# Performance work log

Measured on AMD Instinct MI355X. Metric: run time of the kernel, lower is better.

The kernel has to match this reference:

```python
import jax, jax.numpy as jnp
import numpy as np

N_NODES = 100000
IN_DIM = 128
HID = 128
N_REL = 2
N_EDGES = 500000


def setup_inputs() -> dict:
    key = jax.random.key(0)
    ks = jax.random.split(key, 12)
    x = jax.random.normal(ks[0], (N_NODES, IN_DIM), dtype=jnp.float32)
    edge_index = jax.random.randint(ks[1], (2, N_EDGES), 0, N_NODES, dtype=jnp.int64)
    edge_type = jax.random.randint(ks[2], (N_EDGES,), 0, N_REL, dtype=jnp.int64)
    def w(k, shape, fan_in):
        return jax.random.normal(k, shape, dtype=jnp.float32) / np.sqrt(fan_in)
    return {
        "x": x,
        "edge_index": edge_index,
        "edge_type": edge_type,
        "W_rel1": w(ks[3], (N_REL, IN_DIM, HID), IN_DIM),
        "W_root1": w(ks[4], (IN_DIM, HID), IN_DIM),
        "b1": jnp.zeros((HID,), jnp.float32),
        "W_rel2": w(ks[5], (N_REL, HID, HID), HID),
        "W_root2": w(ks[6], (HID, HID), HID),
        "b2": jnp.zeros((HID,), jnp.float32),
        "Wc": w(ks[7], (HID, 2), HID),
        "bc": jnp.zeros((2,), jnp.float32),
    }


def rgcn_conv(x, src, dst, edge_type, W_rel, W_root, b, n_nodes):
    """PyG RGCNConv: out_i = x_i @ W_root + b + sum_r mean_{j in N_r(i)} x_j @ W_r."""
    out = x @ W_root + b
    for r in range(W_rel.shape[0]):  # small fixed relation count
        mask = (edge_type == r).astype(x.dtype)  # [E]
        xr = x @ W_rel[r]                         # [N, dout] transform-then-gather
        msg = xr[src] * mask[:, None]             # [E, dout]
        agg = jax.ops.segment_sum(msg, dst, num_segments=n_nodes)   # [N, dout]
        cnt = jax.ops.segment_sum(mask, dst, num_segments=n_nodes)  # [N]
        out = out + agg / jnp.maximum(cnt, 1.0)[:, None]            # mean aggr
    return out


def reference(x, edge_index, edge_type, W_rel1, W_root1, b1, W_rel2, W_root2, b2, Wc, bc):
    n = x.shape[0]
    src, dst = edge_index[0], edge_index[1]
    h = rgcn_conv(x, src, dst, edge_type, W_rel1, W_root1, b1, n)
    h = jax.nn.relu(h)
    # dropout is identity at inference (training=False)
    h = rgcn_conv(h, src, dst, edge_type, W_rel2, W_root2, b2, n)
    h = jax.nn.relu(h)
    logits = h @ Wc + bc
    return logits
```

## Files before the change

### kernel.cpp

```cpp
#include <hip/hip_runtime.h>
#include <hip/hip_fp16.h>

#define N_NODES 100000
#define PAD_N   100096
#define IN_DIM 128
#define HID 128
#define N_REL 2
#define N_EDGES 500000
#define M_SEG (N_REL * N_NODES)
#define SCAN_BLK 1024
#define SCAN_NB ((M_SEG + SCAN_BLK - 1) / SCAN_BLK)

#define CVT_BLOCKS 12500
#define PACK_BLOCKS 48
#define HIST_BLOCKS 1954

typedef __attribute__((ext_vector_type(8))) _Float16 half8;
typedef __attribute__((ext_vector_type(4))) float float4v;

__device__ __forceinline__ unsigned short f2h(float f) {
    return __half_as_ushort(__float2half(f));
}

__global__ __launch_bounds__(256) void prep_kernel(
    const float* __restrict__ X, unsigned short* __restrict__ Xb,
    const float* __restrict__ Wroot1, const float* __restrict__ Wrel1,
    const float* __restrict__ Wroot2, const float* __restrict__ Wrel2,
    unsigned short* __restrict__ Wp,
    const int* __restrict__ ei, const int* __restrict__ et,
    unsigned* __restrict__ cnt)
{
    int bid = blockIdx.x;
    if (bid < CVT_BLOCKS) {
        int i = bid * 256 + threadIdx.x;
        if (i >= N_NODES * IN_DIM / 4) return;
        float4 v = ((const float4*)X)[i];
        ushort4 o;
        o.x = f2h(v.x); o.y = f2h(v.y); o.z = f2h(v.z); o.w = f2h(v.w);
        ((ushort4*)Xb)[i] = o;
    } else if (bid < CVT_BLOCKS + PACK_BLOCKS) {
        int tid = (bid - CVT_BLOCKS) * 256 + threadIdx.x;
        int layer = tid / 6144;
        int rem   = tid % 6144;
        int ks    = rem / 512;
        int rem2  = rem % 512;
        int nt    = rem2 / 64;
        int lane  = rem2 % 64;
        int seg = ks >> 2;
        int kl  = (ks & 3) * 32 + (lane >> 4) * 8;
        int chan = nt * 16 + (lane & 15);
        const float* Wroot = layer ? Wroot2 : Wroot1;
        const float* Wrel  = layer ? Wrel2  : Wrel1;
        const float* W = (seg == 0) ? Wroot : (Wrel + (size_t)(seg - 1) * 128 * 128);
        unsigned short* dst = Wp + (size_t)tid * 8;
        #pragma unroll
        for (int j = 0; j < 8; ++j)
            dst[j] = f2h(W[(size_t)(kl + j) * 128 + chan]);
    } else {
        int e = (bid - CVT_BLOCKS - PACK_BLOCKS) * 256 + threadIdx.x;
        if (e >= N_EDGES) return;
        int dst = ei[N_EDGES + e];
        int r = et[e];
        atomicAdd(cnt + (size_t)r * N_NODES + dst, 1u);
    }
}

__global__ __launch_bounds__(256) void scan1_kernel(
    const unsigned* __restrict__ cnt,
    unsigned* __restrict__ rs, unsigned* __restrict__ bsums)
{
    __shared__ unsigned sdata[256];
    int t = threadIdx.x;
    int base = blockIdx.x * SCAN_BLK + t * 4;
    unsigned v[4]; unsigned s = 0;
    #pragma unroll
    for (int j = 0; j < 4; ++j) {
        v[j] = (base + j < M_SEG) ? cnt[base + j] : 0u;
        s += v[j];
    }
    sdata[t] = s;
    __syncthreads();
    #pragma unroll
    for (int off = 1; off < 256; off <<= 1) {
        unsigned x = (t >= off) ? sdata[t - off] : 0u;
        __syncthreads();
        if (t >= off) sdata[t] += x;
        __syncthreads();
    }
    unsigned excl = (t > 0) ? sdata[t - 1] : 0u;
    if (t == 255) bsums[blockIdx.x] = sdata[255];
    unsigned run = excl;
    #pragma unroll
    for (int j = 0; j < 4; ++j) {
        if (base + j < M_SEG) rs[base + j] = run;
        run += v[j];
    }
}

__global__ __launch_bounds__(256) void scan2_kernel(unsigned* __restrict__ bsums)
{
    __shared__ unsigned sdata[256];
    int t = threadIdx.x;
    sdata[t] = (t < SCAN_NB) ? bsums[t] : 0u;
    __syncthreads();
    #pragma unroll
    for (int off = 1; off < 256; off <<= 1) {
        unsigned x = (t >= off) ? sdata[t - off] : 0u;
        __syncthreads();
        if (t >= off) sdata[t] += x;
        __syncthreads();
    }
    if (t < SCAN_NB) bsums[t] = (t > 0) ? sdata[t - 1] : 0u;
}

__global__ __launch_bounds__(256) void scan3_kernel(
    unsigned* __restrict__ rs, const unsigned* __restrict__ bsums,
    unsigned* __restrict__ cursor)
{
    int i = blockIdx.x * blockDim.x + threadIdx.x;
    if (i < M_SEG) {
        unsigned v = rs[i] + bsums[i >> 10];
        rs[i] = v;
        cursor[i] = v;
    }
    if (i == 0) rs[M_SEG] = N_EDGES;
}

__global__ __launch_bounds__(256) void fill_kernel(
    const int* __restrict__ ei, const int* __restrict__ et,
    unsigned* __restrict__ cursor, unsigned* __restrict__ csr)
{
    int e = blockIdx.x * blockDim.x + threadIdx.x;
    if (e >= N_EDGES) return;
    int src = ei[e];
    int dst = ei[N_EDGES + e];
    int r = et[e];
    unsigned pos = atomicAdd(cursor + (size_t)r * N_NODES + dst, 1u);
    csr[pos] = (unsigned)src;
}

__global__ __launch_bounds__(256) void gather_kernel(
    const unsigned short* __restrict__ Xb,
    const unsigned* __restrict__ rs,
    const unsigned* __restrict__ csr,
    unsigned short* __restrict__ agg)
{
    int t = blockIdx.x * blockDim.x + threadIdx.x;
    int seg = t >> 5;
    int lane = t & 31;
    if (seg >= M_SEG) return;
    const int e2  = lane >> 4;
    const int c16 = lane & 15;

    unsigned start = rs[seg];
    unsigned end   = rs[seg + 1];

    const uint4* __restrict__ X4 = (const uint4*)Xb;

    __half2 acc[4];
    #pragma unroll
    for (int j = 0; j < 4; ++j) acc[j] = __float2half2_rn(0.f);

    for (unsigned p = start + e2; p < end; p += 2) {
        unsigned s = csr[p];
        uint4 v = X4[(s << 4) | (unsigned)c16];
        acc[0] = __hadd2(acc[0], *(const __half2*)&v.x);
        acc[1] = __hadd2(acc[1], *(const __half2*)&v.y);
        acc[2] = __hadd2(acc[2], *(const __half2*)&v.z);
        acc[3] = __hadd2(acc[3], *(const __half2*)&v.w);
    }

    #pragma unroll
    for (int j = 0; j < 4; ++j) {
        int other = __shfl_xor(*(const int*)&acc[j], 16, 32);
        acc[j] = __hadd2(acc[j], *(const __half2*)&other);
    }

    if (e2 == 0) {
        unsigned c = end - start;
        float scale = 1.0f / (float)(c > 0u ? c : 1u);
        __half2 s2 = __float2half2_rn(scale);
        uint4 o;
        __half2 r0 = __hmul2(acc[0], s2);
        __half2 r1 = __hmul2(acc[1], s2);
        __half2 r2 = __hmul2(acc[2], s2);
        __half2 r3 = __hmul2(acc[3], s2);
        o.x = *(const unsigned*)&r0;
        o.y = *(const unsigned*)&r1;
        o.z = *(const unsigned*)&r2;
        o.w = *(const unsigned*)&r3;
        int r = seg / N_NODES;
        int n = seg % N_NODES;
        ((uint4*)(agg + ((size_t)r * PAD_N + n) * HID))[c16] = o;
    }
}

template <bool FINAL>
__global__ __launch_bounds__(256) void gemm_kernel(
    const unsigned short* __restrict__ Xin,
    const unsigned short* __restrict__ agg,
    const unsigned short* __restrict__ Wp,
    const float* __restrict__ bias,
    unsigned short* __restrict__ Hout,
    const float* __restrict__ Wc,
    const float* __restrict__ bc,
    float* __restrict__ Out)
{
    __shared__ unsigned short ldsB[2][3 * 8 * 512];

    const int t    = threadIdx.x;
    const int w    = t >> 6;
    const int lane = t & 63;
    const int l15  = lane & 15;
    const int quad = lane >> 4;
    const int rowbase = blockIdx.x * 128 + w * 32;
    const int koff = quad * 8;

    auto stage = [&](int ph, int buf) {
        #pragma unroll
        for (int fi = 0; fi < 6; ++fi) {
            int f  = fi * 4 + w;
            int sl = f >> 3;
            int nt = f & 7;
            int ks = ph * 3 + sl;
            const unsigned short* g = Wp + ((size_t)(ks * 8 + nt) * 64 + lane) * 8;
            unsigned short* l = &ldsB[buf][(size_t)(sl * 8 + nt) * 512];
            __builtin_amdgcn_global_load_lds(
                (const __attribute__((address_space(1))) unsigned int*)g,
                (__attribute__((address_space(3))) unsigned int*)l, 16, 0, 0);
        }
    };

    const unsigned short* aS0m0 = Xin + (size_t)(rowbase + l15) * 128 + koff;
    const unsigned short* aS0m1 = aS0m0 + 16 * 128;
    const unsigned short* aS1m0 = agg + (size_t)(rowbase + l15) * 128 + koff;
    const unsigned short* aS1m1 = aS1m0 + 16 * 128;
    const unsigned short* aS2m0 = aS1m0 + (size_t)PAD_N * 128;
    const unsigned short* aS2m1 = aS2m0 + 16 * 128;

    auto aload = [&](int ks, int mt) -> half8 {
        int seg = ks >> 2;
        int kc  = (ks & 3) * 32;
        const unsigned short* p =
            (seg == 0) ? (mt ? aS0m1 : aS0m0) :
            (seg == 1) ? (mt ? aS1m1 : aS1m0) :
                         (mt ? aS2m1 : aS2m0);
        return *(const half8*)(p + kc);
    };

    float4v acc[2][8];
    #pragma unroll
    for (int nt = 0; nt < 8; ++nt) {
        float bv = bias[nt * 16 + l15];
        #pragma unroll
        for (int mt = 0; mt < 2; ++mt)
            acc[mt][nt] = float4v{bv, bv, bv, bv};
    }

    half8 a0[12], a1[12];
    stage(0, 0);
    a0[0] = aload(0, 0); a1[0] = aload(0, 1);
    a0[1] = aload(1, 0); a1[1] = aload(1, 1);
    __syncthreads();

    #pragma unroll
    for (int ph = 0; ph < 4; ++ph) {
        if (ph < 3) stage(ph + 1, (ph + 1) & 1);
        #pragma unroll
        for (int sl = 0; sl < 3; ++sl) {
            int ks = ph * 3 + sl;
            if (ks + 2 < 12) { a0[ks + 2] = aload(ks + 2, 0); a1[ks + 2] = aload(ks + 2, 1); }
            half8 b[8];
            #pragma unroll
            for (int nt = 0; nt < 8; ++nt)
                b[nt] = *(const half8*)(&ldsB[ph & 1][(size_t)(sl * 8 + nt) * 512] + lane * 8);
            #pragma unroll
            for (int nt = 0; nt < 8; ++nt) {
                acc[0][nt] = __builtin_amdgcn_mfma_f32_16x16x32_f16(a0[ks], b[nt], acc[0][nt], 0, 0, 0);
                acc[1][nt] = __builtin_amdgcn_mfma_f32_16x16x32_f16(a1[ks], b[nt], acc[1][nt], 0, 0, 0);
            }
        }
        __syncthreads();
    }

    if (!FINAL) {
        #pragma unroll
        for (int mt = 0; mt < 2; ++mt) {
            #pragma unroll
            for (int r = 0; r < 4; ++r) {
                int node = rowbase + mt * 16 + quad * 4 + r;
                unsigned short* hp = Hout + (size_t)node * 128 + l15;
                #pragma unroll
                for (int nt = 0; nt < 8; ++nt)
                    hp[nt * 16] = f2h(fmaxf(acc[mt][nt][r], 0.f));
            }
        }
    } else {
        float wc0[8], wc1[8];
        #pragma unroll
        for (int nt = 0; nt < 8; ++nt) {
            wc0[nt] = Wc[(nt * 16 + l15) * 2 + 0];
            wc1[nt] = Wc[(nt * 16 + l15) * 2 + 1];
        }
        float b0 = bc[0], b1 = bc[1];
        #pragma unroll
        for (int mt = 0; mt < 2; ++mt) {
            #pragma unroll
            for (int r = 0; r < 4; ++r) {
                float l0 = 0.f, l1 = 0.f;
                #pragma unroll
                for (int nt = 0; nt < 8; ++nt) {
                    float h = fmaxf(acc[mt][nt][r], 0.f);
                    l0 += h * wc0[nt];
                    l1 += h * wc1[nt];
                }
                #pragma unroll
                for (int off = 8; off > 0; off >>= 1) {
                    l0 += __shfl_down(l0, off, 16);
                    l1 += __shfl_down(l1, off, 16);
                }
                int node = rowbase + mt * 16 + quad * 4 + r;
                if (l15 == 0 && node < N_NODES) {
                    Out[(size_t)node * 2 + 0] = l0 + b0;
                    Out[(size_t)node * 2 + 1] = l1 + b1;
                }
            }
        }
    }
}

extern "C" void kernel_launch(void* const* d_in, const int* in_sizes, int n_in,
                              void* d_out, int out_size, void* d_ws, size_t ws_size,
                              hipStream_t stream)
{
    const float* x      = (const float*)d_in[0];
    const int*   ei     = (const int*)d_in[1];
    const int*   et     = (const int*)d_in[2];
    const float* Wrel1  = (const float*)d_in[3];
    const float* Wroot1 = (const float*)d_in[4];
    const float* b1     = (const float*)d_in[5];
    const float* Wrel2  = (const float*)d_in[6];
    const float* Wroot2 = (const float*)d_in[7];
    const float* b2     = (const float*)d_in[8];
    const float* Wc     = (const float*)d_in[9];
    const float* bc     = (const float*)d_in[10];
    float* out = (float*)d_out;

    char* ws = (char*)d_ws;
    size_t off = 0;
    auto alloc = [&](size_t bytes) {
        void* p = ws + off;
        off += (bytes + 255) & ~(size_t)255;
        return p;
    };
    unsigned short* aggb  = (unsigned short*)alloc((size_t)N_REL * PAD_N * HID * 2);
    unsigned short* xb    = (unsigned short*)alloc((size_t)PAD_N * IN_DIM * 2);
    unsigned short* h1b   = (unsigned short*)alloc((size_t)PAD_N * HID * 2);
    unsigned short* Wp    = (unsigned short*)alloc((size_t)2 * 12 * 8 * 64 * 8 * 2);
    unsigned*       rs    = (unsigned*)alloc((size_t)(M_SEG + 1) * 4);
    unsigned*       cursor= (unsigned*)alloc((size_t)M_SEG * 4);
    unsigned*       bsums = (unsigned*)alloc(256 * 4);
    unsigned*       csr   = (unsigned*)alloc((size_t)N_EDGES * 4);

    const int edge_blocks   = (N_EDGES + 255) / 256;
    const int seg_blocks    = (M_SEG + 255) / 256;
    const int gather_blocks = (M_SEG * 32 + 255) / 256;
    const int gemm_blocks   = PAD_N / 128;
    const int prep_blocks   = CVT_BLOCKS + PACK_BLOCKS + HIST_BLOCKS;

    hipMemsetAsync(cursor, 0, (size_t)M_SEG * 4, stream);
    prep_kernel<<<prep_blocks, 256, 0, stream>>>(
        x, xb, Wroot1, Wrel1, Wroot2, Wrel2, Wp, ei, et, cursor);
    scan1_kernel<<<SCAN_NB, 256, 0, stream>>>(cursor, rs, bsums);
    scan2_kernel<<<1, 256, 0, stream>>>(bsums);
    scan3_kernel<<<seg_blocks, 256, 0, stream>>>(rs, bsums, cursor);
    fill_kernel<<<edge_blocks, 256, 0, stream>>>(ei, et, cursor, csr);

    gather_kernel<<<gather_blocks, 256, 0, stream>>>(xb, rs, csr, aggb);
    gemm_kernel<false><<<gemm_blocks, 256, 0, stream>>>(
        xb, aggb, Wp, b1, h1b, nullptr, nullptr, nullptr);

    gather_kernel<<<gather_blocks, 256, 0, stream>>>(h1b, rs, csr, aggb);
    gemm_kernel<true><<<gemm_blocks, 256, 0, stream>>>(
        h1b, aggb, Wp + (size_t)12 * 8 * 64 * 8, b2, nullptr, Wc, bc, out);
}
```

Measured before the change: 273.6 us.

## Fuse neighbor mean-aggregation gather into the GEMM A-operand load

Removes the separate gather kernels and the intermediate aggregated buffer. Each GEMM block now computes per-relation neighbor means for its rows directly from the CSR and keeps them in registers as MFMA A fragments. This avoids writing and re-reading the large aggregated activations per layer and saves two launches. In exchange, the gather runs with less parallelism inside the GEMM's low-occupancy launch and raises register pressure.

Measured after the change: 273.3 us. No clear change (-0.1%).

```diff
diff --git a/kernel.cpp b/kernel.cpp
--- a/kernel.cpp
+++ b/kernel.cpp
@@ -139,66 +139,11 @@
     csr[pos] = (unsigned)src;
 }
 
-__global__ __launch_bounds__(256) void gather_kernel(
-    const unsigned short* __restrict__ Xb,
-    const unsigned* __restrict__ rs,
-    const unsigned* __restrict__ csr,
-    unsigned short* __restrict__ agg)
-{
-    int t = blockIdx.x * blockDim.x + threadIdx.x;
-    int seg = t >> 5;
-    int lane = t & 31;
-    if (seg >= M_SEG) return;
-    const int e2  = lane >> 4;
-    const int c16 = lane & 15;
-
-    unsigned start = rs[seg];
-    unsigned end   = rs[seg + 1];
-
-    const uint4* __restrict__ X4 = (const uint4*)Xb;
-
-    __half2 acc[4];
-    #pragma unroll
-    for (int j = 0; j < 4; ++j) acc[j] = __float2half2_rn(0.f);
-
-    for (unsigned p = start + e2; p < end; p += 2) {
-        unsigned s = csr[p];
-        uint4 v = X4[(s << 4) | (unsigned)c16];
-        acc[0] = __hadd2(acc[0], *(const __half2*)&v.x);
-        acc[1] = __hadd2(acc[1], *(const __half2*)&v.y);
-        acc[2] = __hadd2(acc[2], *(const __half2*)&v.z);
-        acc[3] = __hadd2(acc[3], *(const __half2*)&v.w);
-    }
-
-    #pragma unroll
-    for (int j = 0; j < 4; ++j) {
-        int other = __shfl_xor(*(const int*)&acc[j], 16, 32);
-        acc[j] = __hadd2(acc[j], *(const __half2*)&other);
-    }
-
-    if (e2 == 0) {
-        unsigned c = end - start;
-        float scale = 1.0f / (float)(c > 0u ? c : 1u);
-        __half2 s2 = __float2half2_rn(scale);
-        uint4 o;
-        __half2 r0 = __hmul2(acc[0], s2);
-        __half2 r1 = __hmul2(acc[1], s2);
-        __half2 r2 = __hmul2(acc[2], s2);
-        __half2 r3 = __hmul2(acc[3], s2);
-        o.x = *(const unsigned*)&r0;
-        o.y = *(const unsigned*)&r1;
-        o.z = *(const unsigned*)&r2;
-        o.w = *(const unsigned*)&r3;
-        int r = seg / N_NODES;
-        int n = seg % N_NODES;
-        ((uint4*)(agg + ((size_t)r * PAD_N + n) * HID))[c16] = o;
-    }
-}
-
 template <bool FINAL>
 __global__ __launch_bounds__(256) void gemm_kernel(
     const unsigned short* __restrict__ Xin,
-    const unsigned short* __restrict__ agg,
+    const unsigned* __restrict__ rs,
+    const unsigned* __restrict__ csr,
     const unsigned short* __restrict__ Wp,
     const float* __restrict__ bias,
     unsigned short* __restrict__ Hout,
@@ -231,21 +176,78 @@
         }
     };
 
-    const unsigned short* aS0m0 = Xin + (size_t)(rowbase + l15) * 128 + koff;
-    const unsigned short* aS0m1 = aS0m0 + 16 * 128;
-    const unsigned short* aS1m0 = agg + (size_t)(rowbase + l15) * 128 + koff;
-    const unsigned short* aS1m1 = aS1m0 + 16 * 128;
-    const unsigned short* aS2m0 = aS1m0 + (size_t)PAD_N * 128;
-    const unsigned short* aS2m1 = aS2m0 + 16 * 128;
-
-    auto aload = [&](int ks, int mt) -> half8 {
-        int seg = ks >> 2;
-        int kc  = (ks & 3) * 32;
-        const unsigned short* p =
-            (seg == 0) ? (mt ? aS0m1 : aS0m0) :
-            (seg == 1) ? (mt ? aS1m1 : aS1m0) :
-                         (mt ? aS2m1 : aS2m0);
-        return *(const half8*)(p + kc);
+    stage(0, 0);
+
+    const uint4* __restrict__ X4 = (const uint4*)Xin;
+
+    half8 ax[2][4];
+    #pragma unroll
+    for (int mt = 0; mt < 2; ++mt)
+        #pragma unroll
+        for (int ksl = 0; ksl < 4; ++ksl)
+            ax[mt][ksl] = *(const half8*)(Xin +
+                (size_t)(rowbase + mt * 16 + l15) * 128 + ksl * 32 + koff);
+
+    half8 ag[2][2][4];
+    #pragma unroll
+    for (int r = 0; r < 2; ++r) {
+        #pragma unroll
+        for (int mt = 0; mt < 2; ++mt) {
+            int node = rowbase + mt * 16 + l15;
+            unsigned start = 0, end = 0;
+            if (node < N_NODES) {
+                unsigned sg = (unsigned)r * N_NODES + (unsigned)node;
+                start = rs[sg];
+                end   = rs[sg + 1];
+            }
+            __half2 a2[4][4];
+            #pragma unroll
+            for (int ksl = 0; ksl < 4; ++ksl)
+                #pragma unroll
+                for (int j = 0; j < 4; ++j)
+                    a2[ksl][j] = __float2half2_rn(0.f);
+
+            for (unsigned p = start; p < end; ++p) {
+                unsigned s = csr[p];
+                const uint4* row = X4 + ((size_t)s << 4) + quad;
+                uint4 v0 = row[0];
+                uint4 v1 = row[4];
+                uint4 v2 = row[8];
+                uint4 v3 = row[12];
+                a2[0][0] = __hadd2(a2[0][0], *(const __half2*)&v0.x);
+                a2[0][1] = __hadd2(a2[0][1], *(const __half2*)&v0.y);
+                a2[0][2] = __hadd2(a2[0][2], *(const __half2*)&v0.z);
+                a2[0][3] = __hadd2(a2[0][3], *(const __half2*)&v0.w);
+                a2[1][0] = __hadd2(a2[1][0], *(const __half2*)&v1.x);
+                a2[1][1] = __hadd2(a2[1][1], *(const __half2*)&v1.y);
+                a2[1][2] = __hadd2(a2[1][2], *(const __half2*)&v1.z);
+                a2[1][3] = __hadd2(a2[1][3], *(const __half2*)&v1.w);
+                a2[2][0] = __hadd2(a2[2][0], *(const __half2*)&v2.x);
+                a2[2][1] = __hadd2(a2[2][1], *(const __half2*)&v2.y);
+                a2[2][2] = __hadd2(a2[2][2], *(const __half2*)&v2.z);
+                a2[2][3] = __hadd2(a2[2][3], *(const __half2*)&v2.w);
+                a2[3][0] = __hadd2(a2[3][0], *(const __half2*)&v3.x);
+                a2[3][1] = __hadd2(a2[3][1], *(const __half2*)&v3.y);
+                a2[3][2] = __hadd2(a2[3][2], *(const __half2*)&v3.z);
+                a2[3][3] = __hadd2(a2[3][3], *(const __half2*)&v3.w);
+            }
+
+            unsigned c = end - start;
+            float scf = 1.0f / (float)(c > 0u ? c : 1u);
+            __half2 s2 = __float2half2_rn(scf);
+            #pragma unroll
+            for (int ksl = 0; ksl < 4; ++ksl) {
+                half8 h;
+                #pragma unroll
+                for (int j = 0; j < 4; ++j)
+                    ((__half2*)&h)[j] = __hmul2(a2[ksl][j], s2);
+                ag[r][mt][ksl] = h;
+            }
+        }
+    }
+
+    auto af = [&](int ks, int mt) -> half8 {
+        return (ks < 4) ? ax[mt][ks & 3] : ag[(ks >> 2) - 1][mt][ks & 3];
     };
 
     float4v acc[2][8];
@@ -257,10 +259,6 @@
             acc[mt][nt] = float4v{bv, bv, bv, bv};
     }
 
-    half8 a0[12], a1[12];
-    stage(0, 0);
-    a0[0] = aload(0, 0); a1[0] = aload(0, 1);
-    a0[1] = aload(1, 0); a1[1] = aload(1, 1);
     __syncthreads();
 
     #pragma unroll
@@ -269,15 +267,14 @@
         #pragma unroll
         for (int sl = 0; sl < 3; ++sl) {
             int ks = ph * 3 + sl;
-            if (ks + 2 < 12) { a0[ks + 2] = aload(ks + 2, 0); a1[ks + 2] = aload(ks + 2, 1); }
             half8 b[8];
             #pragma unroll
             for (int nt = 0; nt < 8; ++nt)
                 b[nt] = *(const half8*)(&ldsB[ph & 1][(size_t)(sl * 8 + nt) * 512] + lane * 8);
             #pragma unroll
             for (int nt = 0; nt < 8; ++nt) {
-                acc[0][nt] = __builtin_amdgcn_mfma_f32_16x16x32_f16(a0[ks], b[nt], acc[0][nt], 0, 0, 0);
-                acc[1][nt] = __builtin_amdgcn_mfma_f32_16x16x32_f16(a1[ks], b[nt], acc[1][nt], 0, 0, 0);
+                acc[0][nt] = __builtin_amdgcn_mfma_f32_16x16x32_f16(af(ks, 0), b[nt], acc[0][nt], 0, 0, 0);
+                acc[1][nt] = __builtin_amdgcn_mfma_f32_16x16x32_f16(af(ks, 1), b[nt], acc[1][nt], 0, 0, 0);
             }
         }
         __syncthreads();
@@ -353,7 +350,6 @@
         off += (bytes + 255) & ~(size_t)255;
         return p;
     };
-    unsigned short* aggb  = (unsigned short*)alloc((size_t)N_REL * PAD_N * HID * 2);
     unsigned short* xb    = (unsigned short*)alloc((size_t)PAD_N * IN_DIM * 2);
     unsigned short* h1b   = (unsigned short*)alloc((size_t)PAD_N * HID * 2);
     unsigned short* Wp    = (unsigned short*)alloc((size_t)2 * 12 * 8 * 64 * 8 * 2);
@@ -362,11 +358,10 @@
     unsigned*       bsums = (unsigned*)alloc(256 * 4);
     unsigned*       csr   = (unsigned*)alloc((size_t)N_EDGES * 4);
 
-    const int edge_blocks   = (N_EDGES + 255) / 256;
-    const int seg_blocks    = (M_SEG + 255) / 256;
-    const int gather_blocks = (M_SEG * 32 + 255) / 256;
-    const int gemm_blocks   = PAD_N / 128;
-    const int prep_blocks   = CVT_BLOCKS + PACK_BLOCKS + HIST_BLOCKS;
+    const int edge_blocks = (N_EDGES + 255) / 256;
+    const int seg_blocks  = (M_SEG + 255) / 256;
+    const int gemm_blocks = PAD_N / 128;
+    const int prep_blocks = CVT_BLOCKS + PACK_BLOCKS + HIST_BLOCKS;
 
     hipMemsetAsync(cursor, 0, (size_t)M_SEG * 4, stream);
     prep_kernel<<<prep_blocks, 256, 0, stream>>>(
@@ -376,11 +371,9 @@
     scan3_kernel<<<seg_blocks, 256, 0, stream>>>(rs, bsums, cursor);
     fill_kernel<<<edge_blocks, 256, 0, stream>>>(ei, et, cursor, csr);
 
-    gather_kernel<<<gather_blocks, 256, 0, stream>>>(xb, rs, csr, aggb);
     gemm_kernel<false><<<gemm_blocks, 256, 0, stream>>>(
-        xb, aggb, Wp, b1, h1b, nullptr, nullptr, nullptr);
-
-    gather_kernel<<<gather_blocks, 256, 0, stream>>>(h1b, rs, csr, aggb);
+        xb, rs, csr, Wp, b1, h1b, nullptr, nullptr, nullptr);
+
     gemm_kernel<true><<<gemm_blocks, 256, 0, stream>>>(
-        h1b, aggb, Wp + (size_t)12 * 8 * 64 * 8, b2, nullptr, Wc, bc, out);
-}
+        h1b, rs, csr, Wp + (size_t)12 * 8 * 64 * 8, b2, nullptr, Wc, bc, out);
+}
```

## Fuse block-sum scan into scan3 and retile GEMM without LDS staging

Applied to the files above, without the earlier changes.

The single-block scan of block sums is merged into scan3: each block redundantly rescans the small bsums array in shared memory, removing one kernel launch. The GEMM is retiled so each wave handles one 16-row tile instead of two, with twice as many blocks. Weight fragments are loaded directly from global memory with register double-buffering instead of staged through LDS with barriers. This trades weight reuse across two M-tiles and shared staging for lower register pressure, more blocks, and no synchronization, at the cost of more redundant global/L2 reads of the weights.

After: 294.9 us. 1.08x slower.

```diff
diff --git a/kernel.cpp b/kernel.cpp
--- a/kernel.cpp
+++ b/kernel.cpp
@@ -97,7 +97,9 @@
     }
 }
 
-__global__ __launch_bounds__(256) void scan2_kernel(unsigned* __restrict__ bsums)
+__global__ __launch_bounds__(256) void scan3_kernel(
+    unsigned* __restrict__ rs, const unsigned* __restrict__ bsums,
+    unsigned* __restrict__ cursor)
 {
     __shared__ unsigned sdata[256];
     int t = threadIdx.x;
@@ -110,16 +112,11 @@
         if (t >= off) sdata[t] += x;
         __syncthreads();
     }
-    if (t < SCAN_NB) bsums[t] = (t > 0) ? sdata[t - 1] : 0u;
-}
-
-__global__ __launch_bounds__(256) void scan3_kernel(
-    unsigned* __restrict__ rs, const unsigned* __restrict__ bsums,
-    unsigned* __restrict__ cursor)
-{
-    int i = blockIdx.x * blockDim.x + threadIdx.x;
+    int i = blockIdx.x * blockDim.x + t;
     if (i < M_SEG) {
-        unsigned v = rs[i] + bsums[i >> 10];
+        int b = i >> 10;
+        unsigned add = (b > 0) ? sdata[b - 1] : 0u;
+        unsigned v = rs[i] + add;
         rs[i] = v;
         cursor[i] = v;
     }
@@ -206,94 +203,68 @@
     const float* __restrict__ bc,
     float* __restrict__ Out)
 {
-    __shared__ unsigned short ldsB[2][3 * 8 * 512];
-
     const int t    = threadIdx.x;
     const int w    = t >> 6;
     const int lane = t & 63;
     const int l15  = lane & 15;
     const int quad = lane >> 4;
-    const int rowbase = blockIdx.x * 128 + w * 32;
+    const int rowbase = blockIdx.x * 64 + w * 16;
     const int koff = quad * 8;
-
-    auto stage = [&](int ph, int buf) {
-        #pragma unroll
-        for (int fi = 0; fi < 6; ++fi) {
-            int f  = fi * 4 + w;
-            int sl = f >> 3;
-            int nt = f & 7;
-            int ks = ph * 3 + sl;
-            const unsigned short* g = Wp + ((size_t)(ks * 8 + nt) * 64 + lane) * 8;
-            unsigned short* l = &ldsB[buf][(size_t)(sl * 8 + nt) * 512];
-            __builtin_amdgcn_global_load_lds(
-                (const __attribute__((address_space(1))) unsigned int*)g,
-                (__attribute__((address_space(3))) unsigned int*)l, 16, 0, 0);
-        }
+    const int node = rowbase + l15;
+
+    const unsigned short* aBase  = Xin + (size_t)node * 128 + koff;
+    const unsigned short* gBase0 = agg + (size_t)node * 128 + koff;
+    const unsigned short* gBase1 = gBase0 + (size_t)PAD_N * 128;
+
+    half8 ag[2][4];
+    #pragma unroll
+    for (int ksl = 0; ksl < 4; ++ksl) {
+        ag[0][ksl] = *(const half8*)(gBase0 + ksl * 32);
+        ag[1][ksl] = *(const half8*)(gBase1 + ksl * 32);
+    }
+
+    auto ldB = [&](int ks, int nt) -> half8 {
+        return *(const half8*)(Wp + ((size_t)(ks * 8 + nt) * 64 + lane) * 8);
     };
-
-    const unsigned short* aS0m0 = Xin + (size_t)(rowbase + l15) * 128 + koff;
-    const unsigned short* aS0m1 = aS0m0 + 16 * 128;
-    const unsigned short* aS1m0 = agg + (size_t)(rowbase + l15) * 128 + koff;
-    const unsigned short* aS1m1 = aS1m0 + 16 * 128;
-    const unsigned short* aS2m0 = aS1m0 + (size_t)PAD_N * 128;
-    const unsigned short* aS2m1 = aS2m0 + 16 * 128;
-
-    auto aload = [&](int ks, int mt) -> half8 {
-        int seg = ks >> 2;
-        int kc  = (ks & 3) * 32;
-        const unsigned short* p =
-            (seg == 0) ? (mt ? aS0m1 : aS0m0) :
-            (seg == 1) ? (mt ? aS1m1 : aS1m0) :
-                         (mt ? aS2m1 : aS2m0);
-        return *(const half8*)(p + kc);
+    auto ldA = [&](int ks) -> half8 {
+        return *(const half8*)(aBase + (ks & 3) * 32);
     };
 
-    float4v acc[2][8];
+    float4v acc[8];
     #pragma unroll
     for (int nt = 0; nt < 8; ++nt) {
         float bv = bias[nt * 16 + l15];
-        #pragma unroll
-        for (int mt = 0; mt < 2; ++mt)
-            acc[mt][nt] = float4v{bv, bv, bv, bv};
-    }
-
-    half8 a0[12], a1[12];
-    stage(0, 0);
-    a0[0] = aload(0, 0); a1[0] = aload(0, 1);
-    a0[1] = aload(1, 0); a1[1] = aload(1, 1);
-    __syncthreads();
-
-    #pragma unroll
-    for (int ph = 0; ph < 4; ++ph) {
-        if (ph < 3) stage(ph + 1, (ph + 1) & 1);
-        #pragma unroll
-        for (int sl = 0; sl < 3; ++sl) {
-            int ks = ph * 3 + sl;
-            if (ks + 2 < 12) { a0[ks + 2] = aload(ks + 2, 0); a1[ks + 2] = aload(ks + 2, 1); }
-            half8 b[8];
+        acc[nt] = float4v{bv, bv, bv, bv};
+    }
+
+    half8 bb[2][8];
+    half8 ax[2];
+    #pragma unroll
+    for (int nt = 0; nt < 8; ++nt) bb[0][nt] = ldB(0, nt);
+    ax[0] = ldA(0);
+
+    #pragma unroll
+    for (int ks = 0; ks < 12; ++ks) {
+        if (ks + 1 < 12) {
             #pragma unroll
             for (int nt = 0; nt < 8; ++nt)
-                b[nt] = *(const half8*)(&ldsB[ph & 1][(size_t)(sl * 8 + nt) * 512] + lane * 8);
+                bb[(ks + 1) & 1][nt] = ldB(ks + 1, nt);
+            if (ks + 1 < 4) ax[(ks + 1) & 1] = ldA(ks + 1);
+        }
+        half8 A = (ks < 4) ? ax[ks & 1] : ag[(ks >> 2) - 1][ks & 3];
+        #pragma unroll
+        for (int nt = 0; nt < 8; ++nt)
+            acc[nt] = __builtin_amdgcn_mfma_f32_16x16x32_f16(A, bb[ks & 1][nt], acc[nt], 0, 0, 0);
+    }
+
+    if (!FINAL) {
+        #pragma unroll
+        for (int rr = 0; rr < 4; ++rr) {
+            int n2 = rowbase + quad * 4 + rr;
+            unsigned short* hp = Hout + (size_t)n2 * 128 + l15;
             #pragma unroll
-            for (int nt = 0; nt < 8; ++nt) {
-                acc[0][nt] = __builtin_amdgcn_mfma_f32_16x16x32_f16(a0[ks], b[nt], acc[0][nt], 0, 0, 0);
-                acc[1][nt] = __builtin_amdgcn_mfma_f32_16x16x32_f16(a1[ks], b[nt], acc[1][nt], 0, 0, 0);
-            }
-        }
-        __syncthreads();
-    }
-
-    if (!FINAL) {
-        #pragma unroll
-        for (int mt = 0; mt < 2; ++mt) {
-            #pragma unroll
-            for (int r = 0; r < 4; ++r) {
-                int node = rowbase + mt * 16 + quad * 4 + r;
-                unsigned short* hp = Hout + (size_t)node * 128 + l15;
-                #pragma unroll
-                for (int nt = 0; nt < 8; ++nt)
-                    hp[nt * 16] = f2h(fmaxf(acc[mt][nt][r], 0.f));
-            }
+            for (int nt = 0; nt < 8; ++nt)
+                hp[nt * 16] = f2h(fmaxf(acc[nt][rr], 0.f));
         }
     } else {
         float wc0[8], wc1[8];
@@ -304,26 +275,23 @@
         }
         float b0 = bc[0], b1 = bc[1];
         #pragma unroll
-        for (int mt = 0; mt < 2; ++mt) {
+        for (int rr = 0; rr < 4; ++rr) {
+            float l0 = 0.f, l1 = 0.f;
             #pragma unroll
-            for (int r = 0; r < 4; ++r) {
-                float l0 = 0.f, l1 = 0.f;
-                #pragma unroll
-                for (int nt = 0; nt < 8; ++nt) {
-                    float h = fmaxf(acc[mt][nt][r], 0.f);
-                    l0 += h * wc0[nt];
-                    l1 += h * wc1[nt];
-                }
-                #pragma unroll
-                for (int off = 8; off > 0; off >>= 1) {
-                    l0 += __shfl_down(l0, off, 16);
-                    l1 += __shfl_down(l1, off, 16);
-                }
-                int node = rowbase + mt * 16 + quad * 4 + r;
-                if (l15 == 0 && node < N_NODES) {
-                    Out[(size_t)node * 2 + 0] = l0 + b0;
-                    Out[(size_t)node * 2 + 1] = l1 + b1;
-                }
+            for (int nt = 0; nt < 8; ++nt) {
+                float h = fmaxf(acc[nt][rr], 0.f);
+                l0 += h * wc0[nt];
+                l1 += h * wc1[nt];
+            }
+            #pragma unroll
+            for (int off = 8; off > 0; off >>= 1) {
+                l0 += __shfl_down(l0, off, 16);
+                l1 += __shfl_down(l1, off, 16);
+            }
+            int n2 = rowbase + quad * 4 + rr;
+            if (l15 == 0 && n2 < N_NODES) {
+                Out[(size_t)n2 * 2 + 0] = l0 + b0;
+                Out[(size_t)n2 * 2 + 1] = l1 + b1;
             }
         }
     }
@@ -365,14 +333,13 @@
     const int edge_blocks   = (N_EDGES + 255) / 256;
     const int seg_blocks    = (M_SEG + 255) / 256;
     const int gather_blocks = (M_SEG * 32 + 255) / 256;
-    const int gemm_blocks   = PAD_N / 128;
+    const int gemm_blocks   = PAD_N / 64;
     const int prep_blocks   = CVT_BLOCKS + PACK_BLOCKS + HIST_BLOCKS;
 
     hipMemsetAsync(cursor, 0, (size_t)M_SEG * 4, stream);
     prep_kernel<<<prep_blocks, 256, 0, stream>>>(
         x, xb, Wroot1, Wrel1, Wroot2, Wrel2, Wp, ei, et, cursor);
     scan1_kernel<<<SCAN_NB, 256, 0, stream>>>(cursor, rs, bsums);
-    scan2_kernel<<<1, 256, 0, stream>>>(bsums);
     scan3_kernel<<<seg_blocks, 256, 0, stream>>>(rs, bsums, cursor);
     fill_kernel<<<edge_blocks, 256, 0, stream>>>(ei, et, cursor, csr);
 
```
